# Optimization experiments

Hardware: AMD Instinct MI355X
Metric: run time of the kernel (lower is better)

## Reference

```python
import jax, jax.numpy as jnp
import numpy as np

NEG_SLOPE = 0.2


def setup_inputs() -> dict:
    key = jax.random.key(0)
    k = jax.random.split(key, 7)
    N, Din, H, D, E = 50000, 256, 8, 32, 1600000
    feat = jax.random.normal(k[0], (N, Din), dtype=jnp.float32)
    W = jax.random.normal(k[1], (Din, H * D), dtype=jnp.float32) * (1.0 / np.sqrt(Din))
    attn_l = jax.random.normal(k[2], (H, D), dtype=jnp.float32) * (1.0 / np.sqrt(D))
    attn_r = jax.random.normal(k[3], (H, D), dtype=jnp.float32) * (1.0 / np.sqrt(D))
    bias = jnp.zeros((H * D,), dtype=jnp.float32)
    src = jax.random.randint(k[4], (E,), 0, N, dtype=jnp.int32)
    dst = jax.random.randint(k[5], (E,), 0, N, dtype=jnp.int32)
    return {"feat": feat, "W": W, "attn_l": attn_l, "attn_r": attn_r,
            "bias": bias, "src": src, "dst": dst}


def reference(feat, W, attn_l, attn_r, bias, src, dst):
    N = feat.shape[0]
    H, D = attn_l.shape
    # linear projection: (N, Din) @ (Din, H*D) -> (N, H, D)
    ft = (feat @ W).reshape(N, H, D)
    # per-node attention logits (N, H)
    el = jnp.einsum('nhd,hd->nh', ft, attn_l)
    er = jnp.einsum('nhd,hd->nh', ft, attn_r)
    # u_add_v on edges, then leaky relu: (E, H)
    e = el[src] + er[dst]
    e = jnp.where(e > 0, e, NEG_SLOPE * e)
    # edge softmax, segmented by destination node
    m = jax.ops.segment_max(e, dst, num_segments=N)        # (N, H)
    ex = jnp.exp(e - m[dst])                               # (E, H)
    s = jax.ops.segment_sum(ex, dst, num_segments=N)       # (N, H)
    a = ex / s[dst]                                        # (E, H)
    # weighted scatter-aggregate: u_mul_e then sum per dst
    msg = ft[src] * a[:, :, None]                          # (E, H, D)
    out = jax.ops.segment_sum(msg, dst, num_segments=N)    # (N, H, D)
    out = out + bias.reshape(1, H, D)
    return out
```

## Files before the change

### kernel.cpp

```cpp
#include <hip/hip_runtime.h>

#define NEG_SLOPE 0.2f
#define LOG2E 1.44269504088896340736f

#define BUK_SHIFT 7
#define BUK_NODES 128
#define BUK_CAP   5120
#define MAX_NBUK  512
#define OVER_CAP  4096

typedef __attribute__((ext_vector_type(8))) short short8v;
typedef __attribute__((ext_vector_type(4))) float float4v;

__device__ __forceinline__ float bf2f(unsigned short u) {
    union { unsigned int u32; float f; } c;
    c.u32 = ((unsigned int)u) << 16;
    return c.f;
}
__device__ __forceinline__ unsigned short f2bf(float f) {
    union { float f; unsigned int u32; } c; c.f = f;
    unsigned int b = c.u32;
    b += 0x7fffu + ((b >> 16) & 1u);
    return (unsigned short)(b >> 16);
}
__device__ __forceinline__ float ub2f(unsigned int d, int b) {
    return (float)((d >> (8 * b)) & 0xffu);
}

__global__ __launch_bounds__(256) void k_init(
    const float* __restrict__ W, unsigned short* __restrict__ wb,
    int* __restrict__ bucket_cnt, int nbuk, int* __restrict__ over_cnt)
{
    if (blockIdx.x < 32) {
        const int t = blockIdx.x * 256 + threadIdx.x;
        const int lane = t & 63;
        const int ct = (t >> 6) & 15;
        const int ks = t >> 10;
        const int col = ct * 16 + (lane & 15);
        const int krow = ks * 32 + (lane >> 4) * 8;
#pragma unroll
        for (int j = 0; j < 8; ++j)
            wb[(size_t)t * 8 + j] = f2bf(W[(krow + j) * 256 + col]);
    } else {
        for (int i = threadIdx.x; i < nbuk; i += 256) bucket_cnt[i] = 0;
        if (threadIdx.x == 0) *over_cnt = 0;
    }
}

__global__ __launch_bounds__(256, 4) void k_gemm(
    const float* __restrict__ A, const unsigned short* __restrict__ wb,
    const float* __restrict__ attn_l, const float* __restrict__ attn_r,
    unsigned char* __restrict__ qft, float* __restrict__ pk,
    float* __restrict__ ers, int M)
{
    __shared__ unsigned short bst[2][8192];
    const int tid = threadIdx.x;
    const int w = tid >> 6, lane = tid & 63;
    const int row0 = blockIdx.x * 64 + w * 16;
    const int arow = row0 + (lane & 15);
    const bool aval = arow < M;
    const float* ap = A + (size_t)arow * 256 + (lane >> 4) * 8;
    const uint4* bsrc = (const uint4*)wb;

    float4v acc[16];
#pragma unroll
    for (int ct = 0; ct < 16; ++ct) acc[ct] = (float4v){0.f, 0.f, 0.f, 0.f};

    uint4 breg0, breg1, breg2, breg3;
    breg0 = bsrc[0 * 256 + tid];
    breg1 = bsrc[1 * 256 + tid];
    breg2 = bsrc[2 * 256 + tid];
    breg3 = bsrc[3 * 256 + tid];
    float4 a0 = make_float4(0.f, 0.f, 0.f, 0.f), a1 = a0;
    if (aval) { a0 = *(const float4*)ap; a1 = *(const float4*)(ap + 4); }
    {
        uint4* d = (uint4*)bst[0];
        d[0 * 256 + tid] = breg0;
        d[1 * 256 + tid] = breg1;
        d[2 * 256 + tid] = breg2;
        d[3 * 256 + tid] = breg3;
    }
    __syncthreads();

    for (int ks = 0; ks < 8; ++ks) {
        const int cur = ks & 1;
        float4 na0 = make_float4(0.f, 0.f, 0.f, 0.f), na1 = na0;
        if (ks < 7) {
            const int u0 = (ks + 1) * 1024 + tid;
            breg0 = bsrc[u0];
            breg1 = bsrc[u0 + 256];
            breg2 = bsrc[u0 + 512];
            breg3 = bsrc[u0 + 768];
            if (aval) {
                na0 = *(const float4*)(ap + (ks + 1) * 32);
                na1 = *(const float4*)(ap + (ks + 1) * 32 + 4);
            }
        }
        short8v ahi, alo;
        {
            float av[8] = {a0.x, a0.y, a0.z, a0.w, a1.x, a1.y, a1.z, a1.w};
#pragma unroll
            for (int j = 0; j < 8; ++j) {
                unsigned short h = f2bf(av[j]);
                ahi[j] = (short)h;
                alo[j] = (short)f2bf(av[j] - bf2f(h));
            }
        }
#pragma unroll
        for (int ct = 0; ct < 16; ++ct) {
            short8v b = *(const short8v*)(&bst[cur][ct * 512 + lane * 8]);
            acc[ct] = __builtin_amdgcn_mfma_f32_16x16x32_bf16(ahi, b, acc[ct], 0, 0, 0);
            acc[ct] = __builtin_amdgcn_mfma_f32_16x16x32_bf16(alo, b, acc[ct], 0, 0, 0);
        }
        if (ks < 7) {
            uint4* d = (uint4*)bst[cur ^ 1];
            d[0 * 256 + tid] = breg0;
            d[1 * 256 + tid] = breg1;
            d[2 * 256 + tid] = breg2;
            d[3 * 256 + tid] = breg3;
            a0 = na0; a1 = na1;
        }
        __syncthreads();
    }

    unsigned char* smq = ((unsigned char*)&bst[0][0]) + (size_t)w * 4224;
    const int c = lane & 15, g = lane >> 4;

#pragma unroll
    for (int reg = 0; reg < 4; ++reg) {
        const int row = row0 + g * 4 + reg;
#pragma unroll
        for (int h = 0; h < 8; ++h) {
            float v0 = acc[2 * h][reg], v1 = acc[2 * h + 1][reg];
            float pl = v0 * attn_l[h * 32 + c] + v1 * attn_l[h * 32 + 16 + c];
            float pr = v0 * attn_r[h * 32 + c] + v1 * attn_r[h * 32 + 16 + c];
            float mx = fmaxf(fabsf(v0), fabsf(v1));
#pragma unroll
            for (int off = 1; off <= 8; off <<= 1) {
                pl += __shfl_xor(pl, off);
                pr += __shfl_xor(pr, off);
                mx = fmaxf(mx, __shfl_xor(mx, off));
            }
            float inv = mx > 0.f ? 127.f / mx : 0.f;
            int q0 = (int)rintf(v0 * inv) + 128;
            int q1 = (int)rintf(v1 * inv) + 128;
            smq[(g * 4 + reg) * 264 + h * 32 + c]      = (unsigned char)q0;
            smq[(g * 4 + reg) * 264 + h * 32 + 16 + c] = (unsigned char)q1;
            if (c == 0 && row < M) {
                pk[(row * 8 + h) * 2]     = pl * LOG2E;
                pk[(row * 8 + h) * 2 + 1] = mx * (1.f / 127.f);
                ers[row * 8 + h]          = pr * LOG2E;
            }
        }
    }
    __syncthreads();
#pragma unroll
    for (int it = 0; it < 16; ++it) {
        int grow = row0 + it;
        if (grow < M)
            *(unsigned int*)(qft + (size_t)grow * 256 + lane * 4) =
                *(const unsigned int*)(smq + it * 264 + lane * 4);
    }
}

__global__ __launch_bounds__(512) void k_bucket(
    const int* __restrict__ src, const int* __restrict__ dst, int E, int nbuk,
    int* __restrict__ bucket_cnt, int2* __restrict__ bucket_edges,
    int* __restrict__ over_cnt, int2* __restrict__ over_edges)
{
    __shared__ int lhist[MAX_NBUK];
    __shared__ int lbase[MAX_NBUK];
    __shared__ int lcur[MAX_NBUK];
    const int tid = threadIdx.x;
    for (int i = tid; i < nbuk; i += 512) lhist[i] = 0;
    __syncthreads();

    const int e0 = blockIdx.x * 4096;
#pragma unroll
    for (int p = 0; p < 8; ++p) {
        int e = e0 + p * 512 + tid;
        if (e < E) atomicAdd(&lhist[dst[e] >> BUK_SHIFT], 1);
    }
    __syncthreads();
    for (int i = tid; i < nbuk; i += 512) {
        int cc = lhist[i];
        lbase[i] = (cc > 0) ? atomicAdd(&bucket_cnt[i], cc) : 0;
        lcur[i] = 0;
    }
    __syncthreads();
#pragma unroll
    for (int p = 0; p < 8; ++p) {
        int e = e0 + p * 512 + tid;
        if (e < E) {
            int d = dst[e];
            int s = src[e];
            int bin = d >> BUK_SHIFT;
            int r = atomicAdd(&lcur[bin], 1);
            int pos = lbase[bin] + r;
            if (pos < BUK_CAP) {
                bucket_edges[(size_t)bin * BUK_CAP + pos] = make_int2(s, d);
            } else {
                int oi = atomicAdd(over_cnt, 1);
                if (oi < OVER_CAP) over_edges[oi] = make_int2(s, d);
            }
        }
    }
}

__global__ __launch_bounds__(256) void k_csr(
    const int2* __restrict__ bucket_edges, const int* __restrict__ bucket_cnt,
    int N, int* __restrict__ deg, int* __restrict__ row_start,
    int* __restrict__ perm_src)
{
    __shared__ int hist[BUK_NODES];
    __shared__ int pfx[BUK_NODES];
    __shared__ int curs[BUK_NODES];
    const int bu = blockIdx.x;
    const int tid = threadIdx.x;
    const int cnt = min(bucket_cnt[bu], BUK_CAP);
    const int node0 = bu << BUK_SHIFT;
    if (tid < BUK_NODES) hist[tid] = 0;
    __syncthreads();
    for (int i = tid; i < cnt; i += 256) {
        int2 ed = bucket_edges[(size_t)bu * BUK_CAP + i];
        atomicAdd(&hist[ed.y & (BUK_NODES - 1)], 1);
    }
    __syncthreads();
    if (tid == 0) {
        int s = 0;
#pragma unroll
        for (int i = 0; i < BUK_NODES; ++i) { pfx[i] = s; s += hist[i]; }
    }
    __syncthreads();
    if (tid < BUK_NODES) {
        int n = node0 + tid;
        if (n < N) {
            deg[n] = hist[tid];
            row_start[n] = bu * BUK_CAP + pfx[tid];
        }
        curs[tid] = pfx[tid];
    }
    __syncthreads();
    for (int i = tid; i < cnt; i += 256) {
        int2 ed = bucket_edges[(size_t)bu * BUK_CAP + i];
        int r = atomicAdd(&curs[ed.y & (BUK_NODES - 1)], 1);
        perm_src[(size_t)bu * BUK_CAP + r] = ed.x;
    }
}

__global__ __launch_bounds__(256) void k_agg(
    const unsigned char* __restrict__ qft,
    const float* __restrict__ pk, const float* __restrict__ ers,
    const int* __restrict__ row_start, const int* __restrict__ deg,
    const int* __restrict__ perm_src,
    const float* __restrict__ bias, float* __restrict__ out, int N,
    const int* __restrict__ over_cnt, const int2* __restrict__ over_edges)
{
    const int tid = threadIdx.x;
    const int lane = tid & 63;
    const int n = blockIdx.x * 4 + (tid >> 6);
    if (n >= N) return;
    const int h = lane >> 3;
    const int slot = lane & 7;
    const int grp = lane & 56;
    const int colb = lane * 4;
    const float erh = ers[(size_t)n * 8 + h];
    const int start = row_start[n];
    const int cnt = deg[n];

    float a0 = 0.f, a1 = 0.f, a2 = 0.f, a3 = 0.f;
    float swb = 0.f;
    float swsb = 0.f;
    float swt = 0.f;
    float swst = 0.f;

    const int nblk = cnt & ~7;
    int j = 0;
    int s_mine = 0;
    if (nblk > 0) s_mine = perm_src[start + slot];
    while (j < nblk) {
        const int s_cur = s_mine;
        j += 8;
        if (j < nblk) s_mine = perm_src[start + j + slot];
        float2 g = *(const float2*)&pk[((size_t)s_cur * 8 + h) * 2];
        float t = g.x + erh;
        t = fmaxf(t, NEG_SLOPE * t);
        float wraw = __builtin_amdgcn_exp2f(t);
        float wsc = wraw * g.y;
        swb += wraw;
        swsb += wsc;
        const int soff = s_cur << 8;
#pragma unroll
        for (int k = 0; k < 8; ++k) {
            int ok = __shfl(soff, grp | k);
            float wk = __shfl(wsc, grp | k);
            unsigned int d = *(const unsigned int*)&qft[(size_t)(ok + colb)];
            a0 = fmaf(wk, ub2f(d, 0), a0);
            a1 = fmaf(wk, ub2f(d, 1), a1);
            a2 = fmaf(wk, ub2f(d, 2), a2);
            a3 = fmaf(wk, ub2f(d, 3), a3);
        }
    }
    for (; j < cnt; ++j) {
        int sv = perm_src[start + j];
        float2 g = *(const float2*)&pk[((size_t)sv * 8 + h) * 2];
        float t = g.x + erh;
        t = fmaxf(t, NEG_SLOPE * t);
        float wraw = __builtin_amdgcn_exp2f(t);
        float wsc = wraw * g.y;
        swt += wraw;
        swst += wsc;
        unsigned int d = *(const unsigned int*)&qft[(size_t)sv * 256 + colb];
        a0 = fmaf(wsc, ub2f(d, 0), a0);
        a1 = fmaf(wsc, ub2f(d, 1), a1);
        a2 = fmaf(wsc, ub2f(d, 2), a2);
        a3 = fmaf(wsc, ub2f(d, 3), a3);
    }

    swb  += __shfl_xor(swb, 1);
    swsb += __shfl_xor(swsb, 1);
    swb  += __shfl_xor(swb, 2);
    swsb += __shfl_xor(swsb, 2);
    swb  += __shfl_xor(swb, 4);
    swsb += __shfl_xor(swsb, 4);
    float swv = swb + swt;
    float sws = swsb + swst;

    int oc = *over_cnt;
    if (oc > 0) {
        oc = min(oc, OVER_CAP);
        for (int i = 0; i < oc; ++i) {
            int2 ed = over_edges[i];
            if (ed.y == n) {
                float2 g = *(const float2*)&pk[((size_t)ed.x * 8 + h) * 2];
                float e = g.x + erh;
                e = e > 0.f ? e : NEG_SLOPE * e;
                float wv = __builtin_amdgcn_exp2f(e);
                float wsx = wv * g.y;
                unsigned int d = *(const unsigned int*)&qft[(size_t)ed.x * 256 + colb];
                a0 = fmaf(wsx, ub2f(d, 0), a0);
                a1 = fmaf(wsx, ub2f(d, 1), a1);
                a2 = fmaf(wsx, ub2f(d, 2), a2);
                a3 = fmaf(wsx, ub2f(d, 3), a3);
                swv += wv;
                sws += wsx;
            }
        }
    }

    float corr = 128.f * sws;
    float inv = swv != 0.f ? 1.f / swv : 0.f;
    float4 b = *(const float4*)&bias[colb];
    float4 o;
    o.x = (a0 - corr) * inv + b.x;
    o.y = (a1 - corr) * inv + b.y;
    o.z = (a2 - corr) * inv + b.z;
    o.w = (a3 - corr) * inv + b.w;
    *(float4*)&out[(size_t)n * 256 + colb] = o;
}

extern "C" void kernel_launch(void* const* d_in, const int* in_sizes, int n_in,
                              void* d_out, int out_size, void* d_ws, size_t ws_size,
                              hipStream_t stream)
{
    const float* feat   = (const float*)d_in[0];
    const float* W      = (const float*)d_in[1];
    const float* attn_l = (const float*)d_in[2];
    const float* attn_r = (const float*)d_in[3];
    const float* bias   = (const float*)d_in[4];
    const int*   src    = (const int*)d_in[5];
    const int*   dst    = (const int*)d_in[6];
    const int N = in_sizes[0] / 256;
    const int E = in_sizes[5];
    const int nbuk = (N + BUK_NODES - 1) >> BUK_SHIFT;
    float* out = (float*)d_out;

    char* ws = (char*)d_ws;
    size_t off = 0;
    auto wsalloc = [&](size_t bytes) -> char* {
        char* p = ws + off;
        off = (off + bytes + 255) & ~(size_t)255;
        return p;
    };
    unsigned char* qft   = (unsigned char*)wsalloc((size_t)N * 256);
    float* pk            = (float*)wsalloc((size_t)N * 16 * 4);
    float* ers           = (float*)wsalloc((size_t)N * 8 * 4);
    int* deg             = (int*)wsalloc((size_t)N * 4);
    int* row_start       = (int*)wsalloc((size_t)N * 4);
    int* bucket_cnt      = (int*)wsalloc((size_t)nbuk * 4);
    int2* bucket_edges   = (int2*)wsalloc((size_t)nbuk * BUK_CAP * 8);
    int* perm_src        = (int*)wsalloc((size_t)nbuk * BUK_CAP * 4);
    int* over_cnt        = (int*)wsalloc(256);
    int2* over_edges     = (int2*)wsalloc((size_t)OVER_CAP * 8);
    unsigned short* wb   = (unsigned short*)wsalloc((size_t)65536 * 2);
    (void)ws_size; (void)n_in; (void)out_size;

    k_init<<<33, 256, 0, stream>>>(W, wb, bucket_cnt, nbuk, over_cnt);
    k_bucket<<<(E + 4095) / 4096, 512, 0, stream>>>(src, dst, E, nbuk,
        bucket_cnt, bucket_edges, over_cnt, over_edges);
    k_gemm<<<(N + 63) / 64, 256, 0, stream>>>(feat, wb, attn_l, attn_r,
        qft, pk, ers, N);
    k_csr<<<nbuk, 256, 0, stream>>>(bucket_edges, bucket_cnt, N, deg, row_start, perm_src);
    k_agg<<<(N + 3) / 4, 256, 0, stream>>>(qft, pk, ers, row_start, deg, perm_src,
        bias, out, N, over_cnt, over_edges);
}
```

Measured before the change: 159.1 us.

## Fuse edge bucketing into GEMM launch, register-cache CSR edges, prefetch pk

Edge bucketing now runs inside the GEMM kernel as extra blocks, so the memory-bound bucketing overlaps the MFMA projection and one launch is dropped. The CSR kernel loads each bucket's edges into registers once (up to 20 per thread) instead of reading bucket_edges twice. The aggregation loop prefetches the next pk pair together with the next source index to hide gather latency. The CSR register arrays raise register pressure, and any edges beyond 20*256 per bucket are silently skipped, although this stays within BUK_CAP.

After: 149.6 us. 1.06x faster.

```diff
diff --git a/kernel.cpp b/kernel.cpp
--- a/kernel.cpp
+++ b/kernel.cpp
@@ -8,6 +8,7 @@
 #define BUK_CAP   5120
 #define MAX_NBUK  512
 #define OVER_CAP  4096
+#define CSR_MAXR  20
 
 typedef __attribute__((ext_vector_type(8))) short short8v;
 typedef __attribute__((ext_vector_type(4))) float float4v;
@@ -47,14 +48,61 @@
     }
 }
 
-__global__ __launch_bounds__(256, 4) void k_gemm(
+__global__ __launch_bounds__(256, 4) void k_fused(
     const float* __restrict__ A, const unsigned short* __restrict__ wb,
     const float* __restrict__ attn_l, const float* __restrict__ attn_r,
     unsigned char* __restrict__ qft, float* __restrict__ pk,
-    float* __restrict__ ers, int M)
+    float* __restrict__ ers, int M,
+    const int* __restrict__ src, const int* __restrict__ dst, int E, int nbuk,
+    int* __restrict__ bucket_cnt, int2* __restrict__ bucket_edges,
+    int* __restrict__ over_cnt, int2* __restrict__ over_edges, int gblocks)
 {
-    __shared__ unsigned short bst[2][8192];
+    __shared__ unsigned char lds_raw[32768];
     const int tid = threadIdx.x;
+
+    if ((int)blockIdx.x >= gblocks) {
+        int* lhist = (int*)lds_raw;
+        int* lbase = lhist + MAX_NBUK;
+        int* lcur  = lhist + 2 * MAX_NBUK;
+        for (int i = tid; i < nbuk; i += 256) lhist[i] = 0;
+        __syncthreads();
+
+        const int e0 = ((int)blockIdx.x - gblocks) * 2048;
+        int es[8], ed[8];
+#pragma unroll
+        for (int p = 0; p < 8; ++p) {
+            int e = e0 + p * 256 + tid;
+            if (e < E) { es[p] = src[e]; ed[p] = dst[e]; }
+            else ed[p] = -1;
+        }
+#pragma unroll
+        for (int p = 0; p < 8; ++p)
+            if (ed[p] >= 0) atomicAdd(&lhist[ed[p] >> BUK_SHIFT], 1);
+        __syncthreads();
+        for (int i = tid; i < nbuk; i += 256) {
+            int cc = lhist[i];
+            lbase[i] = (cc > 0) ? atomicAdd(&bucket_cnt[i], cc) : 0;
+            lcur[i] = 0;
+        }
+        __syncthreads();
+#pragma unroll
+        for (int p = 0; p < 8; ++p) {
+            if (ed[p] >= 0) {
+                int bin = ed[p] >> BUK_SHIFT;
+                int r = atomicAdd(&lcur[bin], 1);
+                int pos = lbase[bin] + r;
+                if (pos < BUK_CAP) {
+                    bucket_edges[(size_t)bin * BUK_CAP + pos] = make_int2(es[p], ed[p]);
+                } else {
+                    int oi = atomicAdd(over_cnt, 1);
+                    if (oi < OVER_CAP) over_edges[oi] = make_int2(es[p], ed[p]);
+                }
+            }
+        }
+        return;
+    }
+
+    unsigned short (*bst)[8192] = (unsigned short(*)[8192])lds_raw;
     const int w = tid >> 6, lane = tid & 63;
     const int row0 = blockIdx.x * 64 + w * 16;
     const int arow = row0 + (lane & 15);
@@ -123,7 +171,7 @@
         __syncthreads();
     }
 
-    unsigned char* smq = ((unsigned char*)&bst[0][0]) + (size_t)w * 4224;
+    unsigned char* smq = lds_raw + (size_t)w * 4224;
     const int c = lane & 15, g = lane >> 4;
 
 #pragma unroll
@@ -160,50 +208,6 @@
         if (grow < M)
             *(unsigned int*)(qft + (size_t)grow * 256 + lane * 4) =
                 *(const unsigned int*)(smq + it * 264 + lane * 4);
-    }
-}
-
-__global__ __launch_bounds__(512) void k_bucket(
-    const int* __restrict__ src, const int* __restrict__ dst, int E, int nbuk,
-    int* __restrict__ bucket_cnt, int2* __restrict__ bucket_edges,
-    int* __restrict__ over_cnt, int2* __restrict__ over_edges)
-{
-    __shared__ int lhist[MAX_NBUK];
-    __shared__ int lbase[MAX_NBUK];
-    __shared__ int lcur[MAX_NBUK];
-    const int tid = threadIdx.x;
-    for (int i = tid; i < nbuk; i += 512) lhist[i] = 0;
-    __syncthreads();
-
-    const int e0 = blockIdx.x * 4096;
-#pragma unroll
-    for (int p = 0; p < 8; ++p) {
-        int e = e0 + p * 512 + tid;
-        if (e < E) atomicAdd(&lhist[dst[e] >> BUK_SHIFT], 1);
-    }
-    __syncthreads();
-    for (int i = tid; i < nbuk; i += 512) {
-        int cc = lhist[i];
-        lbase[i] = (cc > 0) ? atomicAdd(&bucket_cnt[i], cc) : 0;
-        lcur[i] = 0;
-    }
-    __syncthreads();
-#pragma unroll
-    for (int p = 0; p < 8; ++p) {
-        int e = e0 + p * 512 + tid;
-        if (e < E) {
-            int d = dst[e];
-            int s = src[e];
-            int bin = d >> BUK_SHIFT;
-            int r = atomicAdd(&lcur[bin], 1);
-            int pos = lbase[bin] + r;
-            if (pos < BUK_CAP) {
-                bucket_edges[(size_t)bin * BUK_CAP + pos] = make_int2(s, d);
-            } else {
-                int oi = atomicAdd(over_cnt, 1);
-                if (oi < OVER_CAP) over_edges[oi] = make_int2(s, d);
-            }
-        }
     }
 }
 
@@ -221,10 +225,20 @@
     const int node0 = bu << BUK_SHIFT;
     if (tid < BUK_NODES) hist[tid] = 0;
     __syncthreads();
-    for (int i = tid; i < cnt; i += 256) {
-        int2 ed = bucket_edges[(size_t)bu * BUK_CAP + i];
-        atomicAdd(&hist[ed.y & (BUK_NODES - 1)], 1);
-    }
+
+    int esr[CSR_MAXR], edr[CSR_MAXR];
+#pragma unroll
+    for (int r = 0; r < CSR_MAXR; ++r) {
+        int i = tid + r * 256;
+        if (i < cnt) {
+            int2 e = bucket_edges[(size_t)bu * BUK_CAP + i];
+            esr[r] = e.x;
+            edr[r] = e.y & (BUK_NODES - 1);
+        } else edr[r] = -1;
+    }
+#pragma unroll
+    for (int r = 0; r < CSR_MAXR; ++r)
+        if (edr[r] >= 0) atomicAdd(&hist[edr[r]], 1);
     __syncthreads();
     if (tid == 0) {
         int s = 0;
@@ -241,10 +255,12 @@
         curs[tid] = pfx[tid];
     }
     __syncthreads();
-    for (int i = tid; i < cnt; i += 256) {
-        int2 ed = bucket_edges[(size_t)bu * BUK_CAP + i];
-        int r = atomicAdd(&curs[ed.y & (BUK_NODES - 1)], 1);
-        perm_src[(size_t)bu * BUK_CAP + r] = ed.x;
+#pragma unroll
+    for (int r = 0; r < CSR_MAXR; ++r) {
+        if (edr[r] >= 0) {
+            int p = atomicAdd(&curs[edr[r]], 1);
+            perm_src[(size_t)bu * BUK_CAP + p] = esr[r];
+        }
     }
 }
 
@@ -269,20 +285,25 @@
     const int cnt = deg[n];
 
     float a0 = 0.f, a1 = 0.f, a2 = 0.f, a3 = 0.f;
-    float swb = 0.f;
-    float swsb = 0.f;
-    float swt = 0.f;
-    float swst = 0.f;
+    float swb = 0.f, swsb = 0.f;
+    float swt = 0.f, swst = 0.f;
 
     const int nblk = cnt & ~7;
     int j = 0;
     int s_mine = 0;
-    if (nblk > 0) s_mine = perm_src[start + slot];
+    float2 g_mine = make_float2(0.f, 0.f);
+    if (nblk > 0) {
+        s_mine = perm_src[start + slot];
+        g_mine = *(const float2*)&pk[((size_t)s_mine * 8 + h) * 2];
+    }
     while (j < nblk) {
         const int s_cur = s_mine;
+        const float2 g = g_mine;
         j += 8;
-        if (j < nblk) s_mine = perm_src[start + j + slot];
-        float2 g = *(const float2*)&pk[((size_t)s_cur * 8 + h) * 2];
+        if (j < nblk) {
+            s_mine = perm_src[start + j + slot];
+            g_mine = *(const float2*)&pk[((size_t)s_mine * 8 + h) * 2];
+        }
         float t = g.x + erh;
         t = fmaxf(t, NEG_SLOPE * t);
         float wraw = __builtin_amdgcn_exp2f(t);
@@ -395,11 +416,13 @@
     unsigned short* wb   = (unsigned short*)wsalloc((size_t)65536 * 2);
     (void)ws_size; (void)n_in; (void)out_size;
 
+    const int gblocks = (N + 63) / 64;
+    const int bblocks = (E + 2047) / 2048;
+
     k_init<<<33, 256, 0, stream>>>(W, wb, bucket_cnt, nbuk, over_cnt);
-    k_bucket<<<(E + 4095) / 4096, 512, 0, stream>>>(src, dst, E, nbuk,
-        bucket_cnt, bucket_edges, over_cnt, over_edges);
-    k_gemm<<<(N + 63) / 64, 256, 0, stream>>>(feat, wb, attn_l, attn_r,
-        qft, pk, ers, N);
+    k_fused<<<gblocks + bblocks, 256, 0, stream>>>(feat, wb, attn_l, attn_r,
+        qft, pk, ers, N, src, dst, E, nbuk,
+        bucket_cnt, bucket_edges, over_cnt, over_edges, gblocks);
     k_csr<<<nbuk, 256, 0, stream>>>(bucket_edges, bucket_cnt, N, deg, row_start, perm_src);
     k_agg<<<(N + 3) / 4, 256, 0, stream>>>(qft, pk, ers, row_start, deg, perm_src,
         bias, out, N, over_cnt, over_edges);
```
